# Kernel tuning notes

Hardware: AMD Instinct MI355X
Metric: run time of the kernel (lower is better)

## Reference

```python
import jax, jax.numpy as jnp
import numpy as np

N_NODES = 50000
N_EDGES = 800000
D_IN, D_HID, D_OUT = 64, 128, 64


def _glorot(key, fan_in, fan_out):
    lim = (6.0 / (fan_in + fan_out)) ** 0.5
    return jax.random.uniform(key, (fan_in, fan_out), jnp.float32, -lim, lim)


def setup_inputs() -> dict:
    key = jax.random.key(0)
    ks = jax.random.split(key, 10)
    x = jax.random.normal(ks[0], (N_NODES, D_IN), jnp.float32)
    edge_index = jax.random.randint(ks[1], (2, N_EDGES), 0, N_NODES, jnp.int64)
    # GINConv1 MLP: Linear(D_IN->D_HID), ReLU, Linear(D_HID->D_HID)
    W1a = _glorot(ks[2], D_IN, D_HID); b1a = jnp.zeros((D_HID,), jnp.float32)
    W1b = _glorot(ks[3], D_HID, D_HID); b1b = jnp.zeros((D_HID,), jnp.float32)
    # GINConv2 MLP: Linear(D_HID->D_HID), ReLU, Linear(D_HID->D_OUT)
    W2a = _glorot(ks[4], D_HID, D_HID); b2a = jnp.zeros((D_HID,), jnp.float32)
    W2b = _glorot(ks[5], D_HID, D_OUT); b2b = jnp.zeros((D_OUT,), jnp.float32)
    return {"x": x, "edge_index": edge_index,
            "W1a": W1a, "b1a": b1a, "W1b": W1b, "b1b": b1b,
            "W2a": W2a, "b2a": b2a, "W2b": W2b, "b2b": b2b}


def _gin_conv(x, src, dst, Wa, ba, Wb, bb):
    # GIN aggregation (eps = 0): h_i = x_i + sum_{j in N(i)} x_j
    msgs = x[src]                                   # [E, d] gather
    agg = jax.ops.segment_sum(msgs, dst, num_segments=x.shape[0])  # [N, d]
    h = x + agg
    # 2-layer MLP
    h = jax.nn.relu(h @ Wa + ba)
    return h @ Wb + bb


def reference(x, edge_index, W1a, b1a, W1b, b1b, W2a, b2a, W2b, b2b):
    src, dst = edge_index[0], edge_index[1]
    h = jax.nn.relu(_gin_conv(x, src, dst, W1a, b1a, W1b, b1b))
    h = jax.nn.relu(_gin_conv(h, src, dst, W2a, b2a, W2b, b2b))
    return h
```

## Files before the change

kernel.cpp:

```cpp
#include <hip/hip_runtime.h>

#define N_NODES 50000
#define N_EDGES 800000

typedef __attribute__((ext_vector_type(8))) short short8;
typedef __attribute__((ext_vector_type(4))) float floatx4;

static __device__ __forceinline__ unsigned short f2b(float f) {
    unsigned int u = __float_as_uint(f);
    unsigned int r = u + 0x7fffu + ((u >> 16) & 1u);
    return (unsigned short)(r >> 16);
}
static __device__ __forceinline__ unsigned int pk(float a, float b) {
    return (unsigned)f2b(a) | ((unsigned)f2b(b) << 16);
}
static __device__ __forceinline__ float blo(unsigned int u) {
    return __uint_as_float(u << 16);
}
static __device__ __forceinline__ float bhi(unsigned int u) {
    return __uint_as_float(u & 0xffff0000u);
}

__global__ void hist_rank_kernel(const int* __restrict__ dst,
                                 int* __restrict__ deg, int* __restrict__ rank,
                                 int n) {
    int i = blockIdx.x * blockDim.x + threadIdx.x;
    if (i < n) rank[i] = atomicAdd(&deg[dst[i]], 1);
}

__global__ __launch_bounds__(1024) void scanA_kernel(
    const int* __restrict__ deg, int* __restrict__ bsum, int n) {
    __shared__ int s[1024];
    const int tid = threadIdx.x;
    int i = blockIdx.x * 1024 + tid;
    s[tid] = (i < n) ? deg[i] : 0;
    __syncthreads();
    for (int d = 512; d > 0; d >>= 1) {
        if (tid < d) s[tid] += s[tid + d];
        __syncthreads();
    }
    if (tid == 0) bsum[blockIdx.x] = s[0];
}

__global__ __launch_bounds__(1024) void scanC_kernel(
    const int* __restrict__ deg, const int* __restrict__ bsum,
    int* __restrict__ off, int n) {
    __shared__ int s[1024];
    __shared__ int bpref;
    const int tid = threadIdx.x;
    if (tid == 0) {
        int p = 0;
        for (int j = 0; j < blockIdx.x; ++j) p += bsum[j];
        bpref = p;
    }
    const int i = blockIdx.x * 1024 + tid;
    const int v = (i < n) ? deg[i] : 0;
    s[tid] = v;
    __syncthreads();
    for (int d = 1; d < 1024; d <<= 1) {
        int t = (tid >= d) ? s[tid - d] : 0;
        __syncthreads();
        s[tid] += t;
        __syncthreads();
    }
    const int excl = s[tid] - v + bpref;
    if (i < n) {
        off[i] = excl;
        if (i == n - 1) off[n] = excl + v;
    }
}

__global__ void fill_kernel(const int* __restrict__ src,
                            const int* __restrict__ dst,
                            const int* __restrict__ rank,
                            const int* __restrict__ off,
                            unsigned short* __restrict__ nbr, int n) {
    int i = blockIdx.x * blockDim.x + threadIdx.x;
    if (i < n) nbr[off[dst[i]] + rank[i]] = (unsigned short)src[i];
}

__global__ __launch_bounds__(256) void prep_kernel(
    const float* __restrict__ W1a, const float* __restrict__ W1b,
    const float* __restrict__ W2a, const float* __restrict__ W2b,
    const float* __restrict__ x, unsigned short* __restrict__ W1aT,
    unsigned short* __restrict__ W1bT, unsigned short* __restrict__ W2aT,
    unsigned short* __restrict__ W2bT, unsigned short* __restrict__ xb,
    int* __restrict__ deg) {
    int i = blockIdx.x * 256 + threadIdx.x;
    if (i < 8192) {
        int n = i >> 6, k = i & 63;
        W1aT[i] = f2b(W1a[k * 128 + n]);
    } else if (i < 24576) {
        int j = i - 8192, n = j >> 7, k = j & 127;
        W1bT[j] = f2b(W1b[k * 128 + n]);
    } else if (i < 40960) {
        int j = i - 24576, n = j >> 7, k = j & 127;
        W2aT[j] = f2b(W2a[k * 128 + n]);
    } else if (i < 49152) {
        int j = i - 40960, n = j >> 7, k = j & 127;
        W2bT[j] = f2b(W2b[k * 64 + n]);
    } else if (i < 49152 + N_NODES * 16) {
        int j = i - 49152;
        float4 v = ((const float4*)x)[j];
        uint2 o;
        o.x = pk(v.x, v.y);
        o.y = pk(v.z, v.w);
        ((uint2*)xb)[j] = o;
    } else {
        int j = i - (49152 + N_NODES * 16);
        if (j < N_NODES) deg[j] = 0;
    }
}

__global__ __launch_bounds__(256) void gather1_kernel(
    const unsigned short* __restrict__ xb, const int* __restrict__ off,
    const unsigned short* __restrict__ nbr, unsigned short* __restrict__ t1,
    int n_nodes) {
    const int tid = threadIdx.x;
    const int node = blockIdx.x * 16 + (tid >> 4);
    const int c = tid & 15;
    if (node >= n_nodes) return;
    const uint2* xr = (const uint2*)xb;
    const uint2 a = xr[(size_t)node * 16 + c];
    float f0 = blo(a.x), f1 = bhi(a.x), f2 = blo(a.y), f3 = bhi(a.y);
    const int lo = off[node], hi = off[node + 1];
    int j = lo;
    for (; j + 4 <= hi; j += 4) {
        const int s0 = nbr[j], s1 = nbr[j + 1], s2 = nbr[j + 2],
                  s3 = nbr[j + 3];
        const uint2 v0 = xr[(size_t)s0 * 16 + c];
        const uint2 v1 = xr[(size_t)s1 * 16 + c];
        const uint2 v2 = xr[(size_t)s2 * 16 + c];
        const uint2 v3 = xr[(size_t)s3 * 16 + c];
        f0 += (blo(v0.x) + blo(v1.x)) + (blo(v2.x) + blo(v3.x));
        f1 += (bhi(v0.x) + bhi(v1.x)) + (bhi(v2.x) + bhi(v3.x));
        f2 += (blo(v0.y) + blo(v1.y)) + (blo(v2.y) + blo(v3.y));
        f3 += (bhi(v0.y) + bhi(v1.y)) + (bhi(v2.y) + bhi(v3.y));
    }
    for (; j < hi; ++j) {
        const uint2 v = xr[(size_t)nbr[j] * 16 + c];
        f0 += blo(v.x); f1 += bhi(v.x);
        f2 += blo(v.y); f3 += bhi(v.y);
    }
    uint2 o;
    o.x = pk(f0, f1);
    o.y = pk(f2, f3);
    ((uint2*)t1)[(size_t)node * 16 + c] = o;
}

__global__ __launch_bounds__(256) void gather2_kernel(
    const unsigned short* __restrict__ h, const int* __restrict__ off,
    const unsigned short* __restrict__ nbr, unsigned short* __restrict__ t2,
    int n_nodes) {
    const int tid = threadIdx.x;
    const int node = blockIdx.x * 16 + (tid >> 4);
    const int c = tid & 15;
    if (node >= n_nodes) return;
    const uint4* hr = (const uint4*)h;
    const uint4 a = hr[(size_t)node * 16 + c];
    float f0 = blo(a.x), f1 = bhi(a.x), f2 = blo(a.y), f3 = bhi(a.y);
    float f4 = blo(a.z), f5 = bhi(a.z), f6 = blo(a.w), f7 = bhi(a.w);
    const int lo = off[node], hi = off[node + 1];
    int j = lo;
    for (; j + 4 <= hi; j += 4) {
        const int s0 = nbr[j], s1 = nbr[j + 1], s2 = nbr[j + 2],
                  s3 = nbr[j + 3];
        const uint4 v0 = hr[(size_t)s0 * 16 + c];
        const uint4 v1 = hr[(size_t)s1 * 16 + c];
        const uint4 v2 = hr[(size_t)s2 * 16 + c];
        const uint4 v3 = hr[(size_t)s3 * 16 + c];
        f0 += (blo(v0.x) + blo(v1.x)) + (blo(v2.x) + blo(v3.x));
        f1 += (bhi(v0.x) + bhi(v1.x)) + (bhi(v2.x) + bhi(v3.x));
        f2 += (blo(v0.y) + blo(v1.y)) + (blo(v2.y) + blo(v3.y));
        f3 += (bhi(v0.y) + bhi(v1.y)) + (bhi(v2.y) + bhi(v3.y));
        f4 += (blo(v0.z) + blo(v1.z)) + (blo(v2.z) + blo(v3.z));
        f5 += (bhi(v0.z) + bhi(v1.z)) + (bhi(v2.z) + bhi(v3.z));
        f6 += (blo(v0.w) + blo(v1.w)) + (blo(v2.w) + blo(v3.w));
        f7 += (bhi(v0.w) + bhi(v1.w)) + (bhi(v2.w) + bhi(v3.w));
    }
    for (; j < hi; ++j) {
        const uint4 v = hr[(size_t)nbr[j] * 16 + c];
        f0 += blo(v.x); f1 += bhi(v.x); f2 += blo(v.y); f3 += bhi(v.y);
        f4 += blo(v.z); f5 += bhi(v.z); f6 += blo(v.w); f7 += bhi(v.w);
    }
    uint4 o;
    o.x = pk(f0, f1); o.y = pk(f2, f3);
    o.z = pk(f4, f5); o.w = pk(f6, f7);
    ((uint4*)t2)[(size_t)node * 16 + c] = o;
}

template <int DIN, int DH, int DOUT, bool OUT_BF16>
__global__ __launch_bounds__(256) void mlp_mfma_kernel(
    const unsigned short* __restrict__ t, const unsigned short* __restrict__ WaT,
    const float* __restrict__ ba, const unsigned short* __restrict__ WbT,
    const float* __restrict__ bb, void* __restrict__ outp, int n_rows) {
    constexpr int SA = DIN + 16;
    constexpr int SH = DH + 16;
    __shared__ unsigned short tA[64 * SA];
    __shared__ unsigned short hidA[64 * SH];

    const int tid = threadIdx.x;
    const int row0 = blockIdx.x * 64;

    constexpr int CHUNKS = 64 * DIN / 8;
    const uint4* tg = (const uint4*)t;
    for (int i = tid; i < CHUNKS; i += 256) {
        const int row = i / (DIN / 8);
        const int cb = i % (DIN / 8);
        uint4 v = {0u, 0u, 0u, 0u};
        const int gr = row0 + row;
        if (gr < n_rows) v = tg[(size_t)gr * (DIN / 8) + cb];
        *(uint4*)&tA[row * SA + cb * 8] = v;
    }
    __syncthreads();

    const int lane = tid & 63;
    const int wv = tid >> 6;
    const int quad = lane >> 4;
    const int l16 = lane & 15;
    const int m0 = wv * 16;

    short8 a1[DIN / 32];
#pragma unroll
    for (int kk = 0; kk < DIN / 32; ++kk)
        a1[kk] = *(const short8*)&tA[(m0 + l16) * SA + kk * 32 + quad * 8];
#pragma unroll
    for (int nt = 0; nt < DH / 16; ++nt) {
        floatx4 acc = {0.f, 0.f, 0.f, 0.f};
#pragma unroll
        for (int kk = 0; kk < DIN / 32; ++kk) {
            short8 b =
                *(const short8*)&WaT[(nt * 16 + l16) * DIN + kk * 32 + quad * 8];
            acc = __builtin_amdgcn_mfma_f32_16x16x32_bf16(a1[kk], b, acc, 0, 0, 0);
        }
        const float bias = ba[nt * 16 + l16];
#pragma unroll
        for (int r = 0; r < 4; ++r) {
            const float v = fmaxf(acc[r] + bias, 0.f);
            hidA[(m0 + quad * 4 + r) * SH + nt * 16 + l16] = f2b(v);
        }
    }

    short8 a2[DH / 32];
#pragma unroll
    for (int kk = 0; kk < DH / 32; ++kk)
        a2[kk] = *(const short8*)&hidA[(m0 + l16) * SH + kk * 32 + quad * 8];
#pragma unroll
    for (int nt = 0; nt < DOUT / 16; ++nt) {
        floatx4 acc = {0.f, 0.f, 0.f, 0.f};
#pragma unroll
        for (int kk = 0; kk < DH / 32; ++kk) {
            short8 b =
                *(const short8*)&WbT[(nt * 16 + l16) * DH + kk * 32 + quad * 8];
            acc = __builtin_amdgcn_mfma_f32_16x16x32_bf16(a2[kk], b, acc, 0, 0, 0);
        }
        const float bias = bb[nt * 16 + l16];
#pragma unroll
        for (int r = 0; r < 4; ++r) {
            const float v = fmaxf(acc[r] + bias, 0.f);
            const int grow = row0 + m0 + quad * 4 + r;
            if (grow < n_rows) {
                if (OUT_BF16)
                    ((unsigned short*)outp)[(size_t)grow * DOUT + nt * 16 + l16] =
                        f2b(v);
                else
                    ((float*)outp)[(size_t)grow * DOUT + nt * 16 + l16] = v;
            }
        }
    }
}

extern "C" void kernel_launch(void* const* d_in, const int* in_sizes, int n_in,
                              void* d_out, int out_size, void* d_ws,
                              size_t ws_size, hipStream_t stream) {
    const float* x   = (const float*)d_in[0];
    const int*   ei  = (const int*)d_in[1];
    const float* W1a = (const float*)d_in[2];
    const float* b1a = (const float*)d_in[3];
    const float* W1b = (const float*)d_in[4];
    const float* b1b = (const float*)d_in[5];
    const float* W2a = (const float*)d_in[6];
    const float* b2a = (const float*)d_in[7];
    const float* W2b = (const float*)d_in[8];
    const float* b2b = (const float*)d_in[9];
    float* out = (float*)d_out;

    const int* src = ei;
    const int* dst = ei + N_EDGES;

    unsigned short* xb = (unsigned short*)d_ws;
    unsigned short* t1 = xb + (size_t)N_NODES * 64;
    unsigned short* h  = t1 + (size_t)N_NODES * 64;
    unsigned short* t2 = h + (size_t)N_NODES * 128;
    unsigned short* W1aT = t2 + (size_t)N_NODES * 128;
    unsigned short* W1bT = W1aT + 8192;
    unsigned short* W2aT = W1bT + 16384;
    unsigned short* W2bT = W2aT + 16384;
    int* deg  = (int*)(W2bT + 8192);
    int* off  = deg + N_NODES;
    int* bsum = off + N_NODES + 1;
    int* rank = bsum + 64;
    unsigned short* nbr = (unsigned short*)(rank + N_EDGES);

    constexpr int NB = (N_NODES + 1023) / 1024;
    constexpr int PREP_THREADS = 49152 + N_NODES * 16 + N_NODES;

    prep_kernel<<<(PREP_THREADS + 255) / 256, 256, 0, stream>>>(
        W1a, W1b, W2a, W2b, x, W1aT, W1bT, W2aT, W2bT, xb, deg);

    hist_rank_kernel<<<(N_EDGES + 255) / 256, 256, 0, stream>>>(dst, deg, rank,
                                                                N_EDGES);
    scanA_kernel<<<NB, 1024, 0, stream>>>(deg, bsum, N_NODES);
    scanC_kernel<<<NB, 1024, 0, stream>>>(deg, bsum, off, N_NODES);
    fill_kernel<<<(N_EDGES + 255) / 256, 256, 0, stream>>>(src, dst, rank, off,
                                                           nbr, N_EDGES);

    gather1_kernel<<<(N_NODES + 15) / 16, 256, 0, stream>>>(xb, off, nbr, t1,
                                                            N_NODES);
    mlp_mfma_kernel<64, 128, 128, true>
        <<<(N_NODES + 63) / 64, 256, 0, stream>>>(t1, W1aT, b1a, W1bT, b1b, h,
                                                  N_NODES);

    gather2_kernel<<<(N_NODES + 15) / 16, 256, 0, stream>>>(h, off, nbr, t2,
                                                            N_NODES);
    mlp_mfma_kernel<128, 128, 64, false>
        <<<(N_NODES + 63) / 64, 256, 0, stream>>>(t2, W2aT, b2a, W2bT, b2b, out,
                                                  N_NODES);
}
```

Baseline: 239.0 us.

## Fuse CSR build into one cooperative kernel and unroll gathers by eight

Merges the prep, histogram, two-stage scan and fill kernels into a single cooperative kernel that separates its phases with grid-wide syncs, so four kernel launch boundaries disappear. The scan now handles four elements per thread with 256-thread blocks. The neighbor gather loops are also unrolled from four to eight loads per iteration to keep more memory requests in flight. The cost is grid.sync overhead, the requirement that 1024 blocks be co-resident, and higher register pressure in the gathers.

```diff
diff --git a/kernel.cpp b/kernel.cpp
--- a/kernel.cpp
+++ b/kernel.cpp
@@ -1,7 +1,14 @@
 #include <hip/hip_runtime.h>
+#include <hip/hip_cooperative_groups.h>
+
+namespace cg = cooperative_groups;
 
 #define N_NODES 50000
 #define N_EDGES 800000
+#define NB 49
+#define W_ITEMS 49152
+#define X_ITEMS (N_NODES * 16)
+#define PREP_TOTAL (W_ITEMS + X_ITEMS + N_NODES)
 
 typedef __attribute__((ext_vector_type(8))) short short8;
 typedef __attribute__((ext_vector_type(4))) float floatx4;
@@ -21,95 +28,109 @@
     return __uint_as_float(u & 0xffff0000u);
 }
 
-__global__ void hist_rank_kernel(const int* __restrict__ dst,
-                                 int* __restrict__ deg, int* __restrict__ rank,
-                                 int n) {
-    int i = blockIdx.x * blockDim.x + threadIdx.x;
-    if (i < n) rank[i] = atomicAdd(&deg[dst[i]], 1);
-}
-
-__global__ __launch_bounds__(1024) void scanA_kernel(
-    const int* __restrict__ deg, int* __restrict__ bsum, int n) {
-    __shared__ int s[1024];
-    const int tid = threadIdx.x;
-    int i = blockIdx.x * 1024 + tid;
-    s[tid] = (i < n) ? deg[i] : 0;
-    __syncthreads();
-    for (int d = 512; d > 0; d >>= 1) {
-        if (tid < d) s[tid] += s[tid + d];
-        __syncthreads();
-    }
-    if (tid == 0) bsum[blockIdx.x] = s[0];
-}
-
-__global__ __launch_bounds__(1024) void scanC_kernel(
-    const int* __restrict__ deg, const int* __restrict__ bsum,
-    int* __restrict__ off, int n) {
-    __shared__ int s[1024];
-    __shared__ int bpref;
-    const int tid = threadIdx.x;
-    if (tid == 0) {
-        int p = 0;
-        for (int j = 0; j < blockIdx.x; ++j) p += bsum[j];
-        bpref = p;
-    }
-    const int i = blockIdx.x * 1024 + tid;
-    const int v = (i < n) ? deg[i] : 0;
-    s[tid] = v;
-    __syncthreads();
-    for (int d = 1; d < 1024; d <<= 1) {
-        int t = (tid >= d) ? s[tid - d] : 0;
-        __syncthreads();
-        s[tid] += t;
-        __syncthreads();
-    }
-    const int excl = s[tid] - v + bpref;
-    if (i < n) {
-        off[i] = excl;
-        if (i == n - 1) off[n] = excl + v;
-    }
-}
-
-__global__ void fill_kernel(const int* __restrict__ src,
-                            const int* __restrict__ dst,
-                            const int* __restrict__ rank,
-                            const int* __restrict__ off,
-                            unsigned short* __restrict__ nbr, int n) {
-    int i = blockIdx.x * blockDim.x + threadIdx.x;
-    if (i < n) nbr[off[dst[i]] + rank[i]] = (unsigned short)src[i];
-}
-
-__global__ __launch_bounds__(256) void prep_kernel(
-    const float* __restrict__ W1a, const float* __restrict__ W1b,
-    const float* __restrict__ W2a, const float* __restrict__ W2b,
-    const float* __restrict__ x, unsigned short* __restrict__ W1aT,
+__global__ __launch_bounds__(256) void csr_mega_kernel(
+    const float* __restrict__ x, const int* __restrict__ src,
+    const int* __restrict__ dst, const float* __restrict__ W1a,
+    const float* __restrict__ W1b, const float* __restrict__ W2a,
+    const float* __restrict__ W2b, unsigned short* __restrict__ W1aT,
     unsigned short* __restrict__ W1bT, unsigned short* __restrict__ W2aT,
     unsigned short* __restrict__ W2bT, unsigned short* __restrict__ xb,
-    int* __restrict__ deg) {
-    int i = blockIdx.x * 256 + threadIdx.x;
-    if (i < 8192) {
-        int n = i >> 6, k = i & 63;
-        W1aT[i] = f2b(W1a[k * 128 + n]);
-    } else if (i < 24576) {
-        int j = i - 8192, n = j >> 7, k = j & 127;
-        W1bT[j] = f2b(W1b[k * 128 + n]);
-    } else if (i < 40960) {
-        int j = i - 24576, n = j >> 7, k = j & 127;
-        W2aT[j] = f2b(W2a[k * 128 + n]);
-    } else if (i < 49152) {
-        int j = i - 40960, n = j >> 7, k = j & 127;
-        W2bT[j] = f2b(W2b[k * 64 + n]);
-    } else if (i < 49152 + N_NODES * 16) {
-        int j = i - 49152;
-        float4 v = ((const float4*)x)[j];
-        uint2 o;
-        o.x = pk(v.x, v.y);
-        o.y = pk(v.z, v.w);
-        ((uint2*)xb)[j] = o;
-    } else {
-        int j = i - (49152 + N_NODES * 16);
-        if (j < N_NODES) deg[j] = 0;
-    }
+    int* __restrict__ deg, int* __restrict__ off, int* __restrict__ bsum,
+    int* __restrict__ rank, unsigned short* __restrict__ nbr) {
+    cg::grid_group grid = cg::this_grid();
+    const int tid = threadIdx.x;
+    const int bid = blockIdx.x;
+    const int nth = gridDim.x * 256;
+    const int gtid = bid * 256 + tid;
+    __shared__ int sscan[256];
+    __shared__ int sbpref;
+
+    for (int i = gtid; i < PREP_TOTAL; i += nth) {
+        if (i < 8192) {
+            int n = i >> 6, k = i & 63;
+            W1aT[i] = f2b(W1a[k * 128 + n]);
+        } else if (i < 24576) {
+            int j = i - 8192, n = j >> 7, k = j & 127;
+            W1bT[j] = f2b(W1b[k * 128 + n]);
+        } else if (i < 40960) {
+            int j = i - 24576, n = j >> 7, k = j & 127;
+            W2aT[j] = f2b(W2a[k * 128 + n]);
+        } else if (i < 49152) {
+            int j = i - 40960, n = j >> 7, k = j & 127;
+            W2bT[j] = f2b(W2b[k * 64 + n]);
+        } else if (i < 49152 + X_ITEMS) {
+            int j = i - 49152;
+            float4 v = ((const float4*)x)[j];
+            uint2 o;
+            o.x = pk(v.x, v.y);
+            o.y = pk(v.z, v.w);
+            ((uint2*)xb)[j] = o;
+        } else {
+            deg[i - (49152 + X_ITEMS)] = 0;
+        }
+    }
+    grid.sync();
+
+    for (int e = gtid; e < N_EDGES; e += nth)
+        rank[e] = atomicAdd(&deg[dst[e]], 1);
+    grid.sync();
+
+    if (bid < NB) {
+        const int base = bid * 1024 + tid * 4;
+        int s = 0;
+#pragma unroll
+        for (int k = 0; k < 4; ++k) {
+            int i = base + k;
+            if (i < N_NODES) s += deg[i];
+        }
+        sscan[tid] = s;
+        __syncthreads();
+        for (int d = 128; d > 0; d >>= 1) {
+            if (tid < d) sscan[tid] += sscan[tid + d];
+            __syncthreads();
+        }
+        if (tid == 0) bsum[bid] = sscan[0];
+    }
+    grid.sync();
+
+    if (bid < NB) {
+        if (tid == 0) {
+            int p = 0;
+            for (int j = 0; j < bid; ++j) p += bsum[j];
+            sbpref = p;
+        }
+        const int base = bid * 1024 + tid * 4;
+        int v[4];
+        int ls = 0;
+#pragma unroll
+        for (int k = 0; k < 4; ++k) {
+            int i = base + k;
+            v[k] = (i < N_NODES) ? deg[i] : 0;
+            ls += v[k];
+        }
+        sscan[tid] = ls;
+        __syncthreads();
+        for (int d = 1; d < 256; d <<= 1) {
+            int t = (tid >= d) ? sscan[tid - d] : 0;
+            __syncthreads();
+            sscan[tid] += t;
+            __syncthreads();
+        }
+        int run = sbpref + sscan[tid] - ls;
+#pragma unroll
+        for (int k = 0; k < 4; ++k) {
+            int i = base + k;
+            if (i < N_NODES) {
+                off[i] = run;
+                run += v[k];
+                if (i == N_NODES - 1) off[N_NODES] = run;
+            }
+        }
+    }
+    grid.sync();
+
+    for (int e = gtid; e < N_EDGES; e += nth)
+        nbr[off[dst[e]] + rank[e]] = (unsigned short)src[e];
 }
 
 __global__ __launch_bounds__(256) void gather1_kernel(
@@ -125,17 +146,26 @@
     float f0 = blo(a.x), f1 = bhi(a.x), f2 = blo(a.y), f3 = bhi(a.y);
     const int lo = off[node], hi = off[node + 1];
     int j = lo;
-    for (; j + 4 <= hi; j += 4) {
+    for (; j + 8 <= hi; j += 8) {
         const int s0 = nbr[j], s1 = nbr[j + 1], s2 = nbr[j + 2],
-                  s3 = nbr[j + 3];
+                  s3 = nbr[j + 3], s4 = nbr[j + 4], s5 = nbr[j + 5],
+                  s6 = nbr[j + 6], s7 = nbr[j + 7];
         const uint2 v0 = xr[(size_t)s0 * 16 + c];
         const uint2 v1 = xr[(size_t)s1 * 16 + c];
         const uint2 v2 = xr[(size_t)s2 * 16 + c];
         const uint2 v3 = xr[(size_t)s3 * 16 + c];
-        f0 += (blo(v0.x) + blo(v1.x)) + (blo(v2.x) + blo(v3.x));
-        f1 += (bhi(v0.x) + bhi(v1.x)) + (bhi(v2.x) + bhi(v3.x));
-        f2 += (blo(v0.y) + blo(v1.y)) + (blo(v2.y) + blo(v3.y));
-        f3 += (bhi(v0.y) + bhi(v1.y)) + (bhi(v2.y) + bhi(v3.y));
+        const uint2 v4 = xr[(size_t)s4 * 16 + c];
+        const uint2 v5 = xr[(size_t)s5 * 16 + c];
+        const uint2 v6 = xr[(size_t)s6 * 16 + c];
+        const uint2 v7 = xr[(size_t)s7 * 16 + c];
+        f0 += ((blo(v0.x) + blo(v1.x)) + (blo(v2.x) + blo(v3.x))) +
+              ((blo(v4.x) + blo(v5.x)) + (blo(v6.x) + blo(v7.x)));
+        f1 += ((bhi(v0.x) + bhi(v1.x)) + (bhi(v2.x) + bhi(v3.x))) +
+              ((bhi(v4.x) + bhi(v5.x)) + (bhi(v6.x) + bhi(v7.x)));
+        f2 += ((blo(v0.y) + blo(v1.y)) + (blo(v2.y) + blo(v3.y))) +
+              ((blo(v4.y) + blo(v5.y)) + (blo(v6.y) + blo(v7.y)));
+        f3 += ((bhi(v0.y) + bhi(v1.y)) + (bhi(v2.y) + bhi(v3.y))) +
+              ((bhi(v4.y) + bhi(v5.y)) + (bhi(v6.y) + bhi(v7.y)));
     }
     for (; j < hi; ++j) {
         const uint2 v = xr[(size_t)nbr[j] * 16 + c];
@@ -162,21 +192,34 @@
     float f4 = blo(a.z), f5 = bhi(a.z), f6 = blo(a.w), f7 = bhi(a.w);
     const int lo = off[node], hi = off[node + 1];
     int j = lo;
-    for (; j + 4 <= hi; j += 4) {
+    for (; j + 8 <= hi; j += 8) {
         const int s0 = nbr[j], s1 = nbr[j + 1], s2 = nbr[j + 2],
-                  s3 = nbr[j + 3];
+                  s3 = nbr[j + 3], s4 = nbr[j + 4], s5 = nbr[j + 5],
+                  s6 = nbr[j + 6], s7 = nbr[j + 7];
         const uint4 v0 = hr[(size_t)s0 * 16 + c];
         const uint4 v1 = hr[(size_t)s1 * 16 + c];
         const uint4 v2 = hr[(size_t)s2 * 16 + c];
         const uint4 v3 = hr[(size_t)s3 * 16 + c];
-        f0 += (blo(v0.x) + blo(v1.x)) + (blo(v2.x) + blo(v3.x));
-        f1 += (bhi(v0.x) + bhi(v1.x)) + (bhi(v2.x) + bhi(v3.x));
-        f2 += (blo(v0.y) + blo(v1.y)) + (blo(v2.y) + blo(v3.y));
-        f3 += (bhi(v0.y) + bhi(v1.y)) + (bhi(v2.y) + bhi(v3.y));
-        f4 += (blo(v0.z) + blo(v1.z)) + (blo(v2.z) + blo(v3.z));
-        f5 += (bhi(v0.z) + bhi(v1.z)) + (bhi(v2.z) + bhi(v3.z));
-        f6 += (blo(v0.w) + blo(v1.w)) + (blo(v2.w) + blo(v3.w));
-        f7 += (bhi(v0.w) + bhi(v1.w)) + (bhi(v2.w) + bhi(v3.w));
+        const uint4 v4 = hr[(size_t)s4 * 16 + c];
+        const uint4 v5 = hr[(size_t)s5 * 16 + c];
+        const uint4 v6 = hr[(size_t)s6 * 16 + c];
+        const uint4 v7 = hr[(size_t)s7 * 16 + c];
+        f0 += ((blo(v0.x) + blo(v1.x)) + (blo(v2.x) + blo(v3.x))) +
+              ((blo(v4.x) + blo(v5.x)) + (blo(v6.x) + blo(v7.x)));
+        f1 += ((bhi(v0.x) + bhi(v1.x)) + (bhi(v2.x) + bhi(v3.x))) +
+              ((bhi(v4.x) + bhi(v5.x)) + (bhi(v6.x) + bhi(v7.x)));
+        f2 += ((blo(v0.y) + blo(v1.y)) + (blo(v2.y) + blo(v3.y))) +
+              ((blo(v4.y) + blo(v5.y)) + (blo(v6.y) + blo(v7.y)));
+        f3 += ((bhi(v0.y) + bhi(v1.y)) + (bhi(v2.y) + bhi(v3.y))) +
+              ((bhi(v4.y) + bhi(v5.y)) + (bhi(v6.y) + bhi(v7.y)));
+        f4 += ((blo(v0.z) + blo(v1.z)) + (blo(v2.z) + blo(v3.z))) +
+              ((blo(v4.z) + blo(v5.z)) + (blo(v6.z) + blo(v7.z)));
+        f5 += ((bhi(v0.z) + bhi(v1.z)) + (bhi(v2.z) + bhi(v3.z))) +
+              ((bhi(v4.z) + bhi(v5.z)) + (bhi(v6.z) + bhi(v7.z)));
+        f6 += ((blo(v0.w) + blo(v1.w)) + (blo(v2.w) + blo(v3.w))) +
+              ((blo(v4.w) + blo(v5.w)) + (blo(v6.w) + blo(v7.w)));
+        f7 += ((bhi(v0.w) + bhi(v1.w)) + (bhi(v2.w) + bhi(v3.w))) +
+              ((bhi(v4.w) + bhi(v5.w)) + (bhi(v6.w) + bhi(v7.w)));
     }
     for (; j < hi; ++j) {
         const uint4 v = hr[(size_t)nbr[j] * 16 + c];
@@ -302,18 +345,13 @@
     int* rank = bsum + 64;
     unsigned short* nbr = (unsigned short*)(rank + N_EDGES);
 
-    constexpr int NB = (N_NODES + 1023) / 1024;
-    constexpr int PREP_THREADS = 49152 + N_NODES * 16 + N_NODES;
-
-    prep_kernel<<<(PREP_THREADS + 255) / 256, 256, 0, stream>>>(
-        W1a, W1b, W2a, W2b, x, W1aT, W1bT, W2aT, W2bT, xb, deg);
-
-    hist_rank_kernel<<<(N_EDGES + 255) / 256, 256, 0, stream>>>(dst, deg, rank,
-                                                                N_EDGES);
-    scanA_kernel<<<NB, 1024, 0, stream>>>(deg, bsum, N_NODES);
-    scanC_kernel<<<NB, 1024, 0, stream>>>(deg, bsum, off, N_NODES);
-    fill_kernel<<<(N_EDGES + 255) / 256, 256, 0, stream>>>(src, dst, rank, off,
-                                                           nbr, N_EDGES);
+    void* args[] = {(void*)&x,    (void*)&src,  (void*)&dst,  (void*)&W1a,
+                    (void*)&W1b,  (void*)&W2a,  (void*)&W2b,  (void*)&W1aT,
+                    (void*)&W1bT, (void*)&W2aT, (void*)&W2bT, (void*)&xb,
+                    (void*)&deg,  (void*)&off,  (void*)&bsum, (void*)&rank,
+                    (void*)&nbr};
+    hipLaunchCooperativeKernel((const void*)csr_mega_kernel, dim3(1024),
+                               dim3(256), args, 0, stream);
 
     gather1_kernel<<<(N_NODES + 15) / 16, 256, 0, stream>>>(xb, off, nbr, t1,
                                                             N_NODES);
```

Measured after the change: 637.1 us. 167% more time.

## Split gather feature columns across blocks with narrow 4-byte loads

Applied to the files above, without the earlier changes.

Both gather kernels now divide each node's feature row into 8 column slices, each handled by a separate block. Every thread loads one 32-bit word (two bf16 values) per neighbor instead of a 64- or 128-bit vector. The inner loop is unrolled to 8 neighbors to keep more loads in flight. The aim is more parallelism and memory-level concurrency, and possibly better cache locality across column slices, but it multiplies the index reads and loop overhead by 8 and issues narrower, less efficient memory transactions.

```diff
diff --git a/kernel.cpp b/kernel.cpp
--- a/kernel.cpp
+++ b/kernel.cpp
@@ -116,77 +116,80 @@
     const unsigned short* __restrict__ xb, const int* __restrict__ off,
     const unsigned short* __restrict__ nbr, unsigned short* __restrict__ t1,
     int n_nodes) {
-    const int tid = threadIdx.x;
-    const int node = blockIdx.x * 16 + (tid >> 4);
-    const int c = tid & 15;
+    const int s = blockIdx.x & 7;
+    const int tid = threadIdx.x;
+    const int node = (blockIdx.x >> 3) * 64 + (tid >> 2);
+    const int c = tid & 3;
     if (node >= n_nodes) return;
-    const uint2* xr = (const uint2*)xb;
-    const uint2 a = xr[(size_t)node * 16 + c];
-    float f0 = blo(a.x), f1 = bhi(a.x), f2 = blo(a.y), f3 = bhi(a.y);
+    const unsigned int* xr = (const unsigned int*)xb;
+    const int base = s * 4 + c;
+    const unsigned int a = xr[(size_t)node * 32 + base];
+    float f0 = blo(a), f1 = bhi(a);
     const int lo = off[node], hi = off[node + 1];
     int j = lo;
-    for (; j + 4 <= hi; j += 4) {
-        const int s0 = nbr[j], s1 = nbr[j + 1], s2 = nbr[j + 2],
-                  s3 = nbr[j + 3];
-        const uint2 v0 = xr[(size_t)s0 * 16 + c];
-        const uint2 v1 = xr[(size_t)s1 * 16 + c];
-        const uint2 v2 = xr[(size_t)s2 * 16 + c];
-        const uint2 v3 = xr[(size_t)s3 * 16 + c];
-        f0 += (blo(v0.x) + blo(v1.x)) + (blo(v2.x) + blo(v3.x));
-        f1 += (bhi(v0.x) + bhi(v1.x)) + (bhi(v2.x) + bhi(v3.x));
-        f2 += (blo(v0.y) + blo(v1.y)) + (blo(v2.y) + blo(v3.y));
-        f3 += (bhi(v0.y) + bhi(v1.y)) + (bhi(v2.y) + bhi(v3.y));
+    for (; j + 8 <= hi; j += 8) {
+        const int n0 = nbr[j], n1 = nbr[j + 1], n2 = nbr[j + 2],
+                  n3 = nbr[j + 3], n4 = nbr[j + 4], n5 = nbr[j + 5],
+                  n6 = nbr[j + 6], n7 = nbr[j + 7];
+        const unsigned int u0 = xr[(size_t)n0 * 32 + base];
+        const unsigned int u1 = xr[(size_t)n1 * 32 + base];
+        const unsigned int u2 = xr[(size_t)n2 * 32 + base];
+        const unsigned int u3 = xr[(size_t)n3 * 32 + base];
+        const unsigned int u4 = xr[(size_t)n4 * 32 + base];
+        const unsigned int u5 = xr[(size_t)n5 * 32 + base];
+        const unsigned int u6 = xr[(size_t)n6 * 32 + base];
+        const unsigned int u7 = xr[(size_t)n7 * 32 + base];
+        f0 += ((blo(u0) + blo(u1)) + (blo(u2) + blo(u3))) +
+              ((blo(u4) + blo(u5)) + (blo(u6) + blo(u7)));
+        f1 += ((bhi(u0) + bhi(u1)) + (bhi(u2) + bhi(u3))) +
+              ((bhi(u4) + bhi(u5)) + (bhi(u6) + bhi(u7)));
     }
     for (; j < hi; ++j) {
-        const uint2 v = xr[(size_t)nbr[j] * 16 + c];
-        f0 += blo(v.x); f1 += bhi(v.x);
-        f2 += blo(v.y); f3 += bhi(v.y);
-    }
-    uint2 o;
-    o.x = pk(f0, f1);
-    o.y = pk(f2, f3);
-    ((uint2*)t1)[(size_t)node * 16 + c] = o;
+        const unsigned int u = xr[(size_t)nbr[j] * 32 + base];
+        f0 += blo(u);
+        f1 += bhi(u);
+    }
+    ((unsigned int*)t1)[(size_t)node * 32 + base] = pk(f0, f1);
 }
 
 __global__ __launch_bounds__(256) void gather2_kernel(
     const unsigned short* __restrict__ h, const int* __restrict__ off,
     const unsigned short* __restrict__ nbr, unsigned short* __restrict__ t2,
     int n_nodes) {
-    const int tid = threadIdx.x;
-    const int node = blockIdx.x * 16 + (tid >> 4);
-    const int c = tid & 15;
+    const int s = blockIdx.x & 7;
+    const int tid = threadIdx.x;
+    const int node = (blockIdx.x >> 3) * 32 + (tid >> 3);
+    const int c = tid & 7;
     if (node >= n_nodes) return;
-    const uint4* hr = (const uint4*)h;
-    const uint4 a = hr[(size_t)node * 16 + c];
-    float f0 = blo(a.x), f1 = bhi(a.x), f2 = blo(a.y), f3 = bhi(a.y);
-    float f4 = blo(a.z), f5 = bhi(a.z), f6 = blo(a.w), f7 = bhi(a.w);
+    const unsigned int* hr = (const unsigned int*)h;
+    const int base = s * 8 + c;
+    const unsigned int a = hr[(size_t)node * 64 + base];
+    float f0 = blo(a), f1 = bhi(a);
     const int lo = off[node], hi = off[node + 1];
     int j = lo;
-    for (; j + 4 <= hi; j += 4) {
-        const int s0 = nbr[j], s1 = nbr[j + 1], s2 = nbr[j + 2],
-                  s3 = nbr[j + 3];
-        const uint4 v0 = hr[(size_t)s0 * 16 + c];
-        const uint4 v1 = hr[(size_t)s1 * 16 + c];
-        const uint4 v2 = hr[(size_t)s2 * 16 + c];
-        const uint4 v3 = hr[(size_t)s3 * 16 + c];
-        f0 += (blo(v0.x) + blo(v1.x)) + (blo(v2.x) + blo(v3.x));
-        f1 += (bhi(v0.x) + bhi(v1.x)) + (bhi(v2.x) + bhi(v3.x));
-        f2 += (blo(v0.y) + blo(v1.y)) + (blo(v2.y) + blo(v3.y));
-        f3 += (bhi(v0.y) + bhi(v1.y)) + (bhi(v2.y) + bhi(v3.y));
-        f4 += (blo(v0.z) + blo(v1.z)) + (blo(v2.z) + blo(v3.z));
-        f5 += (bhi(v0.z) + bhi(v1.z)) + (bhi(v2.z) + bhi(v3.z));
-        f6 += (blo(v0.w) + blo(v1.w)) + (blo(v2.w) + blo(v3.w));
-        f7 += (bhi(v0.w) + bhi(v1.w)) + (bhi(v2.w) + bhi(v3.w));
+    for (; j + 8 <= hi; j += 8) {
+        const int n0 = nbr[j], n1 = nbr[j + 1], n2 = nbr[j + 2],
+                  n3 = nbr[j + 3], n4 = nbr[j + 4], n5 = nbr[j + 5],
+                  n6 = nbr[j + 6], n7 = nbr[j + 7];
+        const unsigned int u0 = hr[(size_t)n0 * 64 + base];
+        const unsigned int u1 = hr[(size_t)n1 * 64 + base];
+        const unsigned int u2 = hr[(size_t)n2 * 64 + base];
+        const unsigned int u3 = hr[(size_t)n3 * 64 + base];
+        const unsigned int u4 = hr[(size_t)n4 * 64 + base];
+        const unsigned int u5 = hr[(size_t)n5 * 64 + base];
+        const unsigned int u6 = hr[(size_t)n6 * 64 + base];
+        const unsigned int u7 = hr[(size_t)n7 * 64 + base];
+        f0 += ((blo(u0) + blo(u1)) + (blo(u2) + blo(u3))) +
+              ((blo(u4) + blo(u5)) + (blo(u6) + blo(u7)));
+        f1 += ((bhi(u0) + bhi(u1)) + (bhi(u2) + bhi(u3))) +
+              ((bhi(u4) + bhi(u5)) + (bhi(u6) + bhi(u7)));
     }
     for (; j < hi; ++j) {
-        const uint4 v = hr[(size_t)nbr[j] * 16 + c];
-        f0 += blo(v.x); f1 += bhi(v.x); f2 += blo(v.y); f3 += bhi(v.y);
-        f4 += blo(v.z); f5 += bhi(v.z); f6 += blo(v.w); f7 += bhi(v.w);
-    }
-    uint4 o;
-    o.x = pk(f0, f1); o.y = pk(f2, f3);
-    o.z = pk(f4, f5); o.w = pk(f6, f7);
-    ((uint4*)t2)[(size_t)node * 16 + c] = o;
+        const unsigned int u = hr[(size_t)nbr[j] * 64 + base];
+        f0 += blo(u);
+        f1 += bhi(u);
+    }
+    ((unsigned int*)t2)[(size_t)node * 64 + base] = pk(f0, f1);
 }
 
 template <int DIN, int DH, int DOUT, bool OUT_BF16>
@@ -315,14 +318,14 @@
     fill_kernel<<<(N_EDGES + 255) / 256, 256, 0, stream>>>(src, dst, rank, off,
                                                            nbr, N_EDGES);
 
-    gather1_kernel<<<(N_NODES + 15) / 16, 256, 0, stream>>>(xb, off, nbr, t1,
-                                                            N_NODES);
+    gather1_kernel<<<((N_NODES + 63) / 64) * 8, 256, 0, stream>>>(
+        xb, off, nbr, t1, N_NODES);
     mlp_mfma_kernel<64, 128, 128, true>
         <<<(N_NODES + 63) / 64, 256, 0, stream>>>(t1, W1aT, b1a, W1bT, b1b, h,
                                                   N_NODES);
 
-    gather2_kernel<<<(N_NODES + 15) / 16, 256, 0, stream>>>(h, off, nbr, t2,
-                                                            N_NODES);
+    gather2_kernel<<<((N_NODES + 31) / 32) * 8, 256, 0, stream>>>(
+        h, off, nbr, t2, N_NODES);
     mlp_mfma_kernel<128, 128, 64, false>
         <<<(N_NODES + 63) / 64, 256, 0, stream>>>(t2, W2aT, b2a, W2bT, b2b, out,
                                                   N_NODES);
```

Result: slower. 327.3 us (+37.0%).

## Split neighbor gathers across wavefront sub-groups and fuse histogram into prep

Applied to the files above, without the earlier changes.

Each node now gets a full 64-lane wavefront. Lanes are split into sub-groups that walk disjoint neighbor subsets, and the partial sums are combined with cross-lane xor shuffles. The intent is more memory-level parallelism per node, since average degree is about 16. Separately, the degree histogram and rank atomics are folded into the prep kernel, with deg zeroed by a memset, which removes one launch. The cost is four times more blocks, idle lanes on low-degree nodes, and shuffle reduction overhead.

```diff
diff --git a/kernel.cpp b/kernel.cpp
--- a/kernel.cpp
+++ b/kernel.cpp
@@ -21,71 +21,14 @@
     return __uint_as_float(u & 0xffff0000u);
 }
 
-__global__ void hist_rank_kernel(const int* __restrict__ dst,
-                                 int* __restrict__ deg, int* __restrict__ rank,
-                                 int n) {
-    int i = blockIdx.x * blockDim.x + threadIdx.x;
-    if (i < n) rank[i] = atomicAdd(&deg[dst[i]], 1);
-}
-
-__global__ __launch_bounds__(1024) void scanA_kernel(
-    const int* __restrict__ deg, int* __restrict__ bsum, int n) {
-    __shared__ int s[1024];
-    const int tid = threadIdx.x;
-    int i = blockIdx.x * 1024 + tid;
-    s[tid] = (i < n) ? deg[i] : 0;
-    __syncthreads();
-    for (int d = 512; d > 0; d >>= 1) {
-        if (tid < d) s[tid] += s[tid + d];
-        __syncthreads();
-    }
-    if (tid == 0) bsum[blockIdx.x] = s[0];
-}
-
-__global__ __launch_bounds__(1024) void scanC_kernel(
-    const int* __restrict__ deg, const int* __restrict__ bsum,
-    int* __restrict__ off, int n) {
-    __shared__ int s[1024];
-    __shared__ int bpref;
-    const int tid = threadIdx.x;
-    if (tid == 0) {
-        int p = 0;
-        for (int j = 0; j < blockIdx.x; ++j) p += bsum[j];
-        bpref = p;
-    }
-    const int i = blockIdx.x * 1024 + tid;
-    const int v = (i < n) ? deg[i] : 0;
-    s[tid] = v;
-    __syncthreads();
-    for (int d = 1; d < 1024; d <<= 1) {
-        int t = (tid >= d) ? s[tid - d] : 0;
-        __syncthreads();
-        s[tid] += t;
-        __syncthreads();
-    }
-    const int excl = s[tid] - v + bpref;
-    if (i < n) {
-        off[i] = excl;
-        if (i == n - 1) off[n] = excl + v;
-    }
-}
-
-__global__ void fill_kernel(const int* __restrict__ src,
-                            const int* __restrict__ dst,
-                            const int* __restrict__ rank,
-                            const int* __restrict__ off,
-                            unsigned short* __restrict__ nbr, int n) {
-    int i = blockIdx.x * blockDim.x + threadIdx.x;
-    if (i < n) nbr[off[dst[i]] + rank[i]] = (unsigned short)src[i];
-}
-
-__global__ __launch_bounds__(256) void prep_kernel(
+__global__ __launch_bounds__(256) void prep_hist_kernel(
     const float* __restrict__ W1a, const float* __restrict__ W1b,
     const float* __restrict__ W2a, const float* __restrict__ W2b,
-    const float* __restrict__ x, unsigned short* __restrict__ W1aT,
-    unsigned short* __restrict__ W1bT, unsigned short* __restrict__ W2aT,
-    unsigned short* __restrict__ W2bT, unsigned short* __restrict__ xb,
-    int* __restrict__ deg) {
+    const float* __restrict__ x, const int* __restrict__ dst,
+    unsigned short* __restrict__ W1aT, unsigned short* __restrict__ W1bT,
+    unsigned short* __restrict__ W2aT, unsigned short* __restrict__ W2bT,
+    unsigned short* __restrict__ xb, int* __restrict__ deg,
+    int* __restrict__ rank) {
     int i = blockIdx.x * 256 + threadIdx.x;
     if (i < 8192) {
         int n = i >> 6, k = i & 63;
@@ -107,9 +50,60 @@
         o.y = pk(v.z, v.w);
         ((uint2*)xb)[j] = o;
     } else {
-        int j = i - (49152 + N_NODES * 16);
-        if (j < N_NODES) deg[j] = 0;
-    }
+        int e = i - (49152 + N_NODES * 16);
+        if (e < N_EDGES) rank[e] = atomicAdd(&deg[dst[e]], 1);
+    }
+}
+
+__global__ __launch_bounds__(1024) void scanA_kernel(
+    const int* __restrict__ deg, int* __restrict__ bsum, int n) {
+    __shared__ int s[1024];
+    const int tid = threadIdx.x;
+    int i = blockIdx.x * 1024 + tid;
+    s[tid] = (i < n) ? deg[i] : 0;
+    __syncthreads();
+    for (int d = 512; d > 0; d >>= 1) {
+        if (tid < d) s[tid] += s[tid + d];
+        __syncthreads();
+    }
+    if (tid == 0) bsum[blockIdx.x] = s[0];
+}
+
+__global__ __launch_bounds__(1024) void scanC_kernel(
+    const int* __restrict__ deg, const int* __restrict__ bsum,
+    int* __restrict__ off, int n) {
+    __shared__ int s[1024];
+    __shared__ int bpref;
+    const int tid = threadIdx.x;
+    if (tid == 0) {
+        int p = 0;
+        for (int j = 0; j < blockIdx.x; ++j) p += bsum[j];
+        bpref = p;
+    }
+    const int i = blockIdx.x * 1024 + tid;
+    const int v = (i < n) ? deg[i] : 0;
+    s[tid] = v;
+    __syncthreads();
+    for (int d = 1; d < 1024; d <<= 1) {
+        int t = (tid >= d) ? s[tid - d] : 0;
+        __syncthreads();
+        s[tid] += t;
+        __syncthreads();
+    }
+    const int excl = s[tid] - v + bpref;
+    if (i < n) {
+        off[i] = excl;
+        if (i == n - 1) off[n] = excl + v;
+    }
+}
+
+__global__ void fill_kernel(const int* __restrict__ src,
+                            const int* __restrict__ dst,
+                            const int* __restrict__ rank,
+                            const int* __restrict__ off,
+                            unsigned short* __restrict__ nbr, int n) {
+    int i = blockIdx.x * blockDim.x + threadIdx.x;
+    if (i < n) nbr[off[dst[i]] + rank[i]] = (unsigned short)src[i];
 }
 
 __global__ __launch_bounds__(256) void gather1_kernel(
@@ -117,35 +111,51 @@
     const unsigned short* __restrict__ nbr, unsigned short* __restrict__ t1,
     int n_nodes) {
     const int tid = threadIdx.x;
-    const int node = blockIdx.x * 16 + (tid >> 4);
-    const int c = tid & 15;
+    const int lane = tid & 63;
+    const int node = blockIdx.x * 4 + (tid >> 6);
     if (node >= n_nodes) return;
-    const uint2* xr = (const uint2*)xb;
-    const uint2 a = xr[(size_t)node * 16 + c];
-    float f0 = blo(a.x), f1 = bhi(a.x), f2 = blo(a.y), f3 = bhi(a.y);
+    const int sub = lane >> 3;
+    const int c = lane & 7;
+    const uint4* xr = (const uint4*)xb;
+    float f0, f1, f2, f3, f4, f5, f6, f7;
+    {
+        const uint4 a = xr[(size_t)node * 8 + c];
+        const float z = (sub == 0) ? 1.0f : 0.0f;
+        f0 = z * blo(a.x); f1 = z * bhi(a.x);
+        f2 = z * blo(a.y); f3 = z * bhi(a.y);
+        f4 = z * blo(a.z); f5 = z * bhi(a.z);
+        f6 = z * blo(a.w); f7 = z * bhi(a.w);
+    }
     const int lo = off[node], hi = off[node + 1];
-    int j = lo;
-    for (; j + 4 <= hi; j += 4) {
-        const int s0 = nbr[j], s1 = nbr[j + 1], s2 = nbr[j + 2],
-                  s3 = nbr[j + 3];
-        const uint2 v0 = xr[(size_t)s0 * 16 + c];
-        const uint2 v1 = xr[(size_t)s1 * 16 + c];
-        const uint2 v2 = xr[(size_t)s2 * 16 + c];
-        const uint2 v3 = xr[(size_t)s3 * 16 + c];
-        f0 += (blo(v0.x) + blo(v1.x)) + (blo(v2.x) + blo(v3.x));
-        f1 += (bhi(v0.x) + bhi(v1.x)) + (bhi(v2.x) + bhi(v3.x));
-        f2 += (blo(v0.y) + blo(v1.y)) + (blo(v2.y) + blo(v3.y));
-        f3 += (bhi(v0.y) + bhi(v1.y)) + (bhi(v2.y) + bhi(v3.y));
-    }
-    for (; j < hi; ++j) {
-        const uint2 v = xr[(size_t)nbr[j] * 16 + c];
-        f0 += blo(v.x); f1 += bhi(v.x);
-        f2 += blo(v.y); f3 += bhi(v.y);
-    }
-    uint2 o;
-    o.x = pk(f0, f1);
-    o.y = pk(f2, f3);
-    ((uint2*)t1)[(size_t)node * 16 + c] = o;
+    int j = lo + sub;
+    for (; j + 8 < hi; j += 16) {
+        const int n0 = nbr[j];
+        const int n1 = nbr[j + 8];
+        const uint4 v0 = xr[(size_t)n0 * 8 + c];
+        const uint4 v1 = xr[(size_t)n1 * 8 + c];
+        f0 += blo(v0.x) + blo(v1.x); f1 += bhi(v0.x) + bhi(v1.x);
+        f2 += blo(v0.y) + blo(v1.y); f3 += bhi(v0.y) + bhi(v1.y);
+        f4 += blo(v0.z) + blo(v1.z); f5 += bhi(v0.z) + bhi(v1.z);
+        f6 += blo(v0.w) + blo(v1.w); f7 += bhi(v0.w) + bhi(v1.w);
+    }
+    if (j < hi) {
+        const uint4 v = xr[(size_t)nbr[j] * 8 + c];
+        f0 += blo(v.x); f1 += bhi(v.x); f2 += blo(v.y); f3 += bhi(v.y);
+        f4 += blo(v.z); f5 += bhi(v.z); f6 += blo(v.w); f7 += bhi(v.w);
+    }
+#pragma unroll
+    for (int m = 8; m <= 32; m <<= 1) {
+        f0 += __shfl_xor(f0, m, 64); f1 += __shfl_xor(f1, m, 64);
+        f2 += __shfl_xor(f2, m, 64); f3 += __shfl_xor(f3, m, 64);
+        f4 += __shfl_xor(f4, m, 64); f5 += __shfl_xor(f5, m, 64);
+        f6 += __shfl_xor(f6, m, 64); f7 += __shfl_xor(f7, m, 64);
+    }
+    if (sub == 0) {
+        uint4 o;
+        o.x = pk(f0, f1); o.y = pk(f2, f3);
+        o.z = pk(f4, f5); o.w = pk(f6, f7);
+        ((uint4*)t1)[(size_t)node * 8 + c] = o;
+    }
 }
 
 __global__ __launch_bounds__(256) void gather2_kernel(
@@ -153,40 +163,51 @@
     const unsigned short* __restrict__ nbr, unsigned short* __restrict__ t2,
     int n_nodes) {
     const int tid = threadIdx.x;
-    const int node = blockIdx.x * 16 + (tid >> 4);
-    const int c = tid & 15;
+    const int lane = tid & 63;
+    const int node = blockIdx.x * 4 + (tid >> 6);
     if (node >= n_nodes) return;
+    const int sub = lane >> 4;
+    const int c = lane & 15;
     const uint4* hr = (const uint4*)h;
-    const uint4 a = hr[(size_t)node * 16 + c];
-    float f0 = blo(a.x), f1 = bhi(a.x), f2 = blo(a.y), f3 = bhi(a.y);
-    float f4 = blo(a.z), f5 = bhi(a.z), f6 = blo(a.w), f7 = bhi(a.w);
+    float f0, f1, f2, f3, f4, f5, f6, f7;
+    {
+        const uint4 a = hr[(size_t)node * 16 + c];
+        const float z = (sub == 0) ? 1.0f : 0.0f;
+        f0 = z * blo(a.x); f1 = z * bhi(a.x);
+        f2 = z * blo(a.y); f3 = z * bhi(a.y);
+        f4 = z * blo(a.z); f5 = z * bhi(a.z);
+        f6 = z * blo(a.w); f7 = z * bhi(a.w);
+    }
     const int lo = off[node], hi = off[node + 1];
-    int j = lo;
-    for (; j + 4 <= hi; j += 4) {
-        const int s0 = nbr[j], s1 = nbr[j + 1], s2 = nbr[j + 2],
-                  s3 = nbr[j + 3];
-        const uint4 v0 = hr[(size_t)s0 * 16 + c];
-        const uint4 v1 = hr[(size_t)s1 * 16 + c];
-        const uint4 v2 = hr[(size_t)s2 * 16 + c];
-        const uint4 v3 = hr[(size_t)s3 * 16 + c];
-        f0 += (blo(v0.x) + blo(v1.x)) + (blo(v2.x) + blo(v3.x));
-        f1 += (bhi(v0.x) + bhi(v1.x)) + (bhi(v2.x) + bhi(v3.x));
-        f2 += (blo(v0.y) + blo(v1.y)) + (blo(v2.y) + blo(v3.y));
-        f3 += (bhi(v0.y) + bhi(v1.y)) + (bhi(v2.y) + bhi(v3.y));
-        f4 += (blo(v0.z) + blo(v1.z)) + (blo(v2.z) + blo(v3.z));
-        f5 += (bhi(v0.z) + bhi(v1.z)) + (bhi(v2.z) + bhi(v3.z));
-        f6 += (blo(v0.w) + blo(v1.w)) + (blo(v2.w) + blo(v3.w));
-        f7 += (bhi(v0.w) + bhi(v1.w)) + (bhi(v2.w) + bhi(v3.w));
-    }
-    for (; j < hi; ++j) {
+    int j = lo + sub;
+    for (; j + 4 < hi; j += 8) {
+        const int n0 = nbr[j];
+        const int n1 = nbr[j + 4];
+        const uint4 v0 = hr[(size_t)n0 * 16 + c];
+        const uint4 v1 = hr[(size_t)n1 * 16 + c];
+        f0 += blo(v0.x) + blo(v1.x); f1 += bhi(v0.x) + bhi(v1.x);
+        f2 += blo(v0.y) + blo(v1.y); f3 += bhi(v0.y) + bhi(v1.y);
+        f4 += blo(v0.z) + blo(v1.z); f5 += bhi(v0.z) + bhi(v1.z);
+        f6 += blo(v0.w) + blo(v1.w); f7 += bhi(v0.w) + bhi(v1.w);
+    }
+    if (j < hi) {
         const uint4 v = hr[(size_t)nbr[j] * 16 + c];
         f0 += blo(v.x); f1 += bhi(v.x); f2 += blo(v.y); f3 += bhi(v.y);
         f4 += blo(v.z); f5 += bhi(v.z); f6 += blo(v.w); f7 += bhi(v.w);
     }
-    uint4 o;
-    o.x = pk(f0, f1); o.y = pk(f2, f3);
-    o.z = pk(f4, f5); o.w = pk(f6, f7);
-    ((uint4*)t2)[(size_t)node * 16 + c] = o;
+#pragma unroll
+    for (int m = 16; m <= 32; m <<= 1) {
+        f0 += __shfl_xor(f0, m, 64); f1 += __shfl_xor(f1, m, 64);
+        f2 += __shfl_xor(f2, m, 64); f3 += __shfl_xor(f3, m, 64);
+        f4 += __shfl_xor(f4, m, 64); f5 += __shfl_xor(f5, m, 64);
+        f6 += __shfl_xor(f6, m, 64); f7 += __shfl_xor(f7, m, 64);
+    }
+    if (sub == 0) {
+        uint4 o;
+        o.x = pk(f0, f1); o.y = pk(f2, f3);
+        o.z = pk(f4, f5); o.w = pk(f6, f7);
+        ((uint4*)t2)[(size_t)node * 16 + c] = o;
+    }
 }
 
 template <int DIN, int DH, int DOUT, bool OUT_BF16>
@@ -303,26 +324,25 @@
     unsigned short* nbr = (unsigned short*)(rank + N_EDGES);
 
     constexpr int NB = (N_NODES + 1023) / 1024;
-    constexpr int PREP_THREADS = 49152 + N_NODES * 16 + N_NODES;
-
-    prep_kernel<<<(PREP_THREADS + 255) / 256, 256, 0, stream>>>(
-        W1a, W1b, W2a, W2b, x, W1aT, W1bT, W2aT, W2bT, xb, deg);
-
-    hist_rank_kernel<<<(N_EDGES + 255) / 256, 256, 0, stream>>>(dst, deg, rank,
-                                                                N_EDGES);
+    constexpr int PREP_THREADS = 49152 + N_NODES * 16 + N_EDGES;
+
+    hipMemsetAsync(deg, 0, N_NODES * sizeof(int), stream);
+    prep_hist_kernel<<<(PREP_THREADS + 255) / 256, 256, 0, stream>>>(
+        W1a, W1b, W2a, W2b, x, dst, W1aT, W1bT, W2aT, W2bT, xb, deg, rank);
+
     scanA_kernel<<<NB, 1024, 0, stream>>>(deg, bsum, N_NODES);
     scanC_kernel<<<NB, 1024, 0, stream>>>(deg, bsum, off, N_NODES);
     fill_kernel<<<(N_EDGES + 255) / 256, 256, 0, stream>>>(src, dst, rank, off,
                                                            nbr, N_EDGES);
 
-    gather1_kernel<<<(N_NODES + 15) / 16, 256, 0, stream>>>(xb, off, nbr, t1,
-                                                            N_NODES);
+    gather1_kernel<<<(N_NODES + 3) / 4, 256, 0, stream>>>(xb, off, nbr, t1,
+                                                          N_NODES);
     mlp_mfma_kernel<64, 128, 128, true>
         <<<(N_NODES + 63) / 64, 256, 0, stream>>>(t1, W1aT, b1a, W1bT, b1b, h,
                                                   N_NODES);
 
-    gather2_kernel<<<(N_NODES + 15) / 16, 256, 0, stream>>>(h, off, nbr, t2,
-                                                            N_NODES);
+    gather2_kernel<<<(N_NODES + 3) / 4, 256, 0, stream>>>(h, off, nbr, t2,
+                                                          N_NODES);
     mlp_mfma_kernel<128, 128, 64, false>
         <<<(N_NODES + 63) / 64, 256, 0, stream>>>(t2, W2aT, b2a, W2bT, b2b, out,
                                                   N_NODES);
```

Measured after the change: 241.4 us. About the same (+1.0%).
